# Kernel optimization log

Measured on AMD Instinct MI355X. Metric: run time of the kernel, lower is better.

## Reference

```python
import jax, jax.numpy as jnp
import numpy as np

D_MODEL = 1024
H = 16
D_K = D_MODEL // H


def setup_inputs() -> dict:
    key = jax.random.key(0)
    ks = jax.random.split(key, 11)
    B, S = 4, 2048
    scale = 1.0 / np.sqrt(D_MODEL)
    inp = {
        "q": jax.random.normal(ks[0], (B, S, D_MODEL), jnp.float32),
        "k": jax.random.normal(ks[1], (B, S, D_MODEL), jnp.float32),
        "v": jax.random.normal(ks[2], (B, S, D_MODEL), jnp.float32),
        "wq": jax.random.normal(ks[3], (D_MODEL, D_MODEL), jnp.float32) * scale,
        "bq": jax.random.normal(ks[4], (D_MODEL,), jnp.float32) * 0.02,
        "wk": jax.random.normal(ks[5], (D_MODEL, D_MODEL), jnp.float32) * scale,
        "bk": jax.random.normal(ks[6], (D_MODEL,), jnp.float32) * 0.02,
        "wv": jax.random.normal(ks[7], (D_MODEL, D_MODEL), jnp.float32) * scale,
        "bv": jax.random.normal(ks[8], (D_MODEL,), jnp.float32) * 0.02,
        "wo": jax.random.normal(ks[9], (D_MODEL, D_MODEL), jnp.float32) * scale,
        "bo": jax.random.normal(ks[10], (D_MODEL,), jnp.float32) * 0.02,
    }
    return inp


def _split_heads(x):
    b, s, d = x.shape
    return x.reshape(b, s, H, D_K).transpose(0, 2, 1, 3)  # b h s k


def reference(q, k, v, wq, bq, wk, bk, wv, bv, wo, bo):
    # linear projections (torch Linear: x @ W^T + b; here weights stored as [in,out])
    qh = _split_heads(q @ wq + bq)
    kh = _split_heads(k @ wk + bk)
    vh = _split_heads(v @ wv + bv)
    scores = jnp.einsum('bhsk,bhtk->bhst', qh, kh) / np.sqrt(D_K)
    attn = jax.nn.softmax(scores, axis=-1)
    wv_ = jnp.einsum('bhst,bhtk->bhsk', attn, vh)
    b, h, s, dk = wv_.shape
    cv = wv_.transpose(0, 2, 1, 3).reshape(b, s, h * dk)
    return cv @ wo + bo
```

## Files before the change

kernel.cpp:

```cpp
#include <hip/hip_runtime.h>


#define DM 1024
#define SQL 2048

typedef __attribute__((ext_vector_type(4))) float floatx4;
typedef __attribute__((ext_vector_type(16))) float floatx16;
typedef __attribute__((ext_vector_type(8))) __bf16 bf16x8;
typedef __attribute__((ext_vector_type(4))) __bf16 bf16x4;

#define SW(row, chunk) (((row) << 6) + ((((chunk) ^ ((row) & 7))) << 3))

#define GLD(gaddr, laddr)                                                              \
  __builtin_amdgcn_global_load_lds(                                                    \
      (const __attribute__((address_space(1))) unsigned int*)(gaddr),                  \
      (__attribute__((address_space(3))) unsigned int*)(laddr), 16, 0, 0)

__device__ __forceinline__ unsigned short f2bf(float f) {
  unsigned int u = __float_as_uint(f);
  u += 0x7fffu + ((u >> 16) & 1u);
  return (unsigned short)(u >> 16);
}

__device__ __forceinline__ unsigned int pack_bf(float lo, float hi) {
  unsigned int a = __float_as_uint(lo) + 0x8000u;
  unsigned int b = __float_as_uint(hi) + 0x8000u;
  return __builtin_amdgcn_perm(b, a, 0x07060302u);
}

__global__ __launch_bounds__(256) void transpose4_kernel(
    const float* __restrict__ w0, const float* __restrict__ w1,
    const float* __restrict__ w2, const float* __restrict__ w3,
    unsigned short* __restrict__ t0, unsigned short* __restrict__ t1,
    unsigned short* __restrict__ t2, unsigned short* __restrict__ t3) {
  __shared__ unsigned short t[64][65];
  int z = blockIdx.z;
  const float* W = (z == 0) ? w0 : (z == 1) ? w1 : (z == 2) ? w2 : w3;
  unsigned short* Wt = (z == 0) ? t0 : (z == 1) ? t1 : (z == 2) ? t2 : t3;
  int tid = threadIdx.x;
  int n0 = blockIdx.x * 64, k0 = blockIdx.y * 64;
  for (int u = 0; u < 16; u++) {
    int idx = u * 256 + tid;
    int k = idx >> 6, n = idx & 63;
    t[k][n] = f2bf(W[(size_t)(k0 + k) * DM + n0 + n]);
  }
  __syncthreads();
  for (int u = 0; u < 16; u++) {
    int idx = u * 256 + tid;
    int n = idx >> 6, k = idx & 63;
    Wt[(size_t)(n0 + n) * DM + k0 + k] = t[k][n];
  }
}

__global__ __launch_bounds__(256) void convert3_kernel(
    const float* __restrict__ s0, const float* __restrict__ s1,
    const float* __restrict__ s2, unsigned short* __restrict__ d0,
    unsigned short* __restrict__ d1, unsigned short* __restrict__ d2) {
  int z = blockIdx.y;
  const float* S = (z == 0) ? s0 : (z == 1) ? s1 : s2;
  unsigned short* D = (z == 0) ? d0 : (z == 1) ? d1 : d2;
  int t = blockIdx.x * 256 + threadIdx.x;
  for (int u = 0; u < 8; u++) {
    int i = (u << 18) + t;
    float4 vv = ((const float4*)S)[i];
    uint2 p;
    p.x = pack_bf(vv.x, vv.y);
    p.y = pack_bf(vv.z, vv.w);
    ((uint2*)D)[i] = p;
  }
}

__device__ __forceinline__ void gemm_core_256x128(
    const unsigned short* __restrict__ A, const unsigned short* __restrict__ Bt,
    int m0, int n0, unsigned short* lds_a, unsigned short* lds_b,
    floatx4 acc[4][4]) {
  int tid = threadIdx.x;
  int wave = tid >> 6, lane = tid & 63;
  int quad = lane >> 4, c16 = lane & 15;
  int wm = wave >> 1, wn = wave & 1;
  int r8 = lane >> 3, l8 = lane & 7;
  int xch = (l8 ^ r8) << 3;

  int r7 = c16 & 7;
  int aoff0 = ((wm * 64 + c16) << 6) + ((quad ^ r7) << 3);
  int aoff1 = ((wm * 64 + c16) << 6) + (((4 + quad) ^ r7) << 3);
  int boff0 = ((wn * 64 + c16) << 6) + ((quad ^ r7) << 3);
  int boff1 = ((wn * 64 + c16) << 6) + (((4 + quad) ^ r7) << 3);

  int aq = wave * 4;
  int bq = wave * 2;

#define STG_A(bufp, kt, u) \
  GLD(&A[(size_t)(m0 + (aq + (u)) * 8 + r8) * DM + (kt) + xch], (bufp) + (aq + (u)) * 512)
#define STG_B(bufp, kt, u) \
  GLD(&Bt[(size_t)(n0 + (bq + (u)) * 8 + r8) * DM + (kt) + xch], (bufp) + (bq + (u)) * 512)

  const floatx4 fz = {0.f, 0.f, 0.f, 0.f};
#pragma unroll
  for (int i = 0; i < 4; i++)
#pragma unroll
    for (int j = 0; j < 4; j++) acc[i][j] = fz;

#pragma unroll
  for (int u = 0; u < 4; u++) STG_A(lds_a, 0, u);
  STG_B(lds_b, 0, 0);
  STG_B(lds_b, 0, 1);
#pragma unroll
  for (int u = 0; u < 4; u++) STG_A(lds_a + 16384, 64, u);
  STG_B(lds_b + 8192, 64, 0);
  STG_B(lds_b + 8192, 64, 1);

  int cur = 0;
#pragma unroll 1
  for (int t = 0; t < 16; ++t) {
    if (t < 15) asm volatile("s_waitcnt vmcnt(6)\n\ts_barrier" ::: "memory");
    else        asm volatile("s_waitcnt vmcnt(0)\n\ts_barrier" ::: "memory");

    const unsigned short* la = lds_a + cur * 16384;
    const unsigned short* lb = lds_b + cur * 8192;
    int stg = cur + 2;
    if (stg >= 3) stg -= 3;
    unsigned short* sa = lds_a + stg * 16384;
    unsigned short* sb = lds_b + stg * 8192;
    bool do_st = (t < 14);
    int kt2 = (t + 2) << 6;

    bf16x8 a_[2], b0[4], b1[4];

    a_[0] = *(const bf16x8*)&la[aoff0];
    a_[1] = *(const bf16x8*)&la[aoff0 + 1024];
    b0[0] = *(const bf16x8*)&lb[boff0];
    b0[1] = *(const bf16x8*)&lb[boff0 + 1024];
    b0[2] = *(const bf16x8*)&lb[boff0 + 2048];
    b0[3] = *(const bf16x8*)&lb[boff0 + 3072];
    if (do_st) { STG_A(sa, kt2, 0); STG_A(sa, kt2, 1); }
    __builtin_amdgcn_s_barrier();
    __builtin_amdgcn_s_setprio(1);
#pragma unroll
    for (int j = 0; j < 4; j++)
      acc[0][j] = __builtin_amdgcn_mfma_f32_16x16x32_bf16(a_[0], b0[j], acc[0][j], 0, 0, 0);
#pragma unroll
    for (int j = 0; j < 4; j++)
      acc[1][j] = __builtin_amdgcn_mfma_f32_16x16x32_bf16(a_[1], b0[j], acc[1][j], 0, 0, 0);
    __builtin_amdgcn_s_setprio(0);
    __builtin_amdgcn_s_barrier();

    a_[0] = *(const bf16x8*)&la[aoff0 + 2048];
    a_[1] = *(const bf16x8*)&la[aoff0 + 3072];
    if (do_st) { STG_A(sa, kt2, 2); STG_A(sa, kt2, 3); }
    __builtin_amdgcn_s_barrier();
    __builtin_amdgcn_s_setprio(1);
#pragma unroll
    for (int j = 0; j < 4; j++)
      acc[2][j] = __builtin_amdgcn_mfma_f32_16x16x32_bf16(a_[0], b0[j], acc[2][j], 0, 0, 0);
#pragma unroll
    for (int j = 0; j < 4; j++)
      acc[3][j] = __builtin_amdgcn_mfma_f32_16x16x32_bf16(a_[1], b0[j], acc[3][j], 0, 0, 0);
    __builtin_amdgcn_s_setprio(0);
    __builtin_amdgcn_s_barrier();

    a_[0] = *(const bf16x8*)&la[aoff1];
    a_[1] = *(const bf16x8*)&la[aoff1 + 1024];
    b1[0] = *(const bf16x8*)&lb[boff1];
    b1[1] = *(const bf16x8*)&lb[boff1 + 1024];
    b1[2] = *(const bf16x8*)&lb[boff1 + 2048];
    b1[3] = *(const bf16x8*)&lb[boff1 + 3072];
    if (do_st) { STG_B(sb, kt2, 0); STG_B(sb, kt2, 1); }
    __builtin_amdgcn_s_barrier();
    __builtin_amdgcn_s_setprio(1);
#pragma unroll
    for (int j = 0; j < 4; j++)
      acc[0][j] = __builtin_amdgcn_mfma_f32_16x16x32_bf16(a_[0], b1[j], acc[0][j], 0, 0, 0);
#pragma unroll
    for (int j = 0; j < 4; j++)
      acc[1][j] = __builtin_amdgcn_mfma_f32_16x16x32_bf16(a_[1], b1[j], acc[1][j], 0, 0, 0);
    __builtin_amdgcn_s_setprio(0);
    __builtin_amdgcn_s_barrier();

    a_[0] = *(const bf16x8*)&la[aoff1 + 2048];
    a_[1] = *(const bf16x8*)&la[aoff1 + 3072];
    __builtin_amdgcn_s_barrier();
    __builtin_amdgcn_s_setprio(1);
#pragma unroll
    for (int j = 0; j < 4; j++)
      acc[2][j] = __builtin_amdgcn_mfma_f32_16x16x32_bf16(a_[0], b1[j], acc[2][j], 0, 0, 0);
#pragma unroll
    for (int j = 0; j < 4; j++)
      acc[3][j] = __builtin_amdgcn_mfma_f32_16x16x32_bf16(a_[1], b1[j], acc[3][j], 0, 0, 0);
    __builtin_amdgcn_s_setprio(0);

    cur = cur + 1;
    if (cur >= 3) cur = 0;
  }
#undef STG_A
#undef STG_B
}

__global__ __launch_bounds__(512, 2) void gemm_qkv_kernel(
    const unsigned short* __restrict__ Aq, const unsigned short* __restrict__ Ak,
    const unsigned short* __restrict__ Av, const unsigned short* __restrict__ wqt,
    const unsigned short* __restrict__ wkt, const unsigned short* __restrict__ wvt,
    const float* __restrict__ bq, const float* __restrict__ bk,
    const float* __restrict__ bv, unsigned short* __restrict__ Qb,
    unsigned short* __restrict__ Kb, unsigned short* __restrict__ VtOut,
    float qscale) {
  __shared__ unsigned short lds_a[3 * 256 * 64];
  __shared__ unsigned short lds_b[3 * 128 * 64];

  int lin = blockIdx.x + (blockIdx.y << 3) + (blockIdx.z << 8);
  int swz = (lin & 7) * 96 + (lin >> 3);
  int z = swz >> 8, rem = swz & 255;
  int m0 = (rem >> 3) << 8;
  int n0 = (rem & 7) << 7;

  const unsigned short* A  = (z == 0) ? Aq : (z == 1) ? Ak : Av;
  const unsigned short* Bt = (z == 0) ? wqt : (z == 1) ? wkt : wvt;
  const float* bias = (z == 0) ? bq : (z == 1) ? bk : bv;

  floatx4 acc[4][4];
  gemm_core_256x128(A, Bt, m0, n0, lds_a, lds_b, acc);

  int tid = threadIdx.x;
  int wave = tid >> 6, lane = tid & 63;
  int quad = lane >> 4, c16 = lane & 15;
  int wm = wave >> 1, wn = wave & 1;

  float scale = (z == 0) ? qscale : 1.0f;
#pragma unroll
  for (int i = 0; i < 4; i++)
#pragma unroll
    for (int j = 0; j < 4; j++) {
      int gc = n0 + wn * 64 + j * 16 + c16;
      float bvv = bias[gc];
      float val[4];
#pragma unroll
      for (int r = 0; r < 4; r++) val[r] = (acc[i][j][r] + bvv) * scale;
      int gr0 = m0 + wm * 64 + i * 16 + quad * 4;
      if (z < 2) {
        unsigned short* O = (z == 0) ? Qb : Kb;
#pragma unroll
        for (int r = 0; r < 4; r++) O[(size_t)(gr0 + r) * DM + gc] = f2bf(val[r]);
      } else {
        int hh = gc >> 6, dd = gc & 63;
        int bidx = gr0 >> 11, srow = gr0 & 2047;
        int s6 = srow & 63;
        int c6 = (s6 & 51) | ((s6 & 4) << 1) | ((s6 & 8) >> 1);
        int srowp = (srow & ~63) | c6;
        uint2 pk;
        pk.x = pack_bf(val[0], val[1]);
        pk.y = pack_bf(val[2], val[3]);
        *(uint2*)&VtOut[((size_t)(bidx * 16 + hh) * 64 + dd) * SQL + srowp] = pk;
      }
    }
}

__global__ __launch_bounds__(512, 2) void gemm_out_kernel(
    const unsigned short* __restrict__ A, const unsigned short* __restrict__ Bt,
    const float* __restrict__ bias, float* __restrict__ O) {
  __shared__ unsigned short lds_a[3 * 256 * 64];
  __shared__ unsigned short lds_b[3 * 128 * 64];

  int lin = blockIdx.x + (blockIdx.y << 3);
  int swz = (lin & 7) * 32 + (lin >> 3);
  int m0 = (swz >> 3) << 8;
  int n0 = (swz & 7) << 7;

  floatx4 acc[4][4];
  gemm_core_256x128(A, Bt, m0, n0, lds_a, lds_b, acc);

  int tid = threadIdx.x;
  int wave = tid >> 6, lane = tid & 63;
  int quad = lane >> 4, c16 = lane & 15;
  int wm = wave >> 1, wn = wave & 1;

#pragma unroll
  for (int i = 0; i < 4; i++)
#pragma unroll
    for (int j = 0; j < 4; j++) {
      int gc = n0 + wn * 64 + j * 16 + c16;
      float bvv = bias[gc];
      int gr0 = m0 + wm * 64 + i * 16 + quad * 4;
#pragma unroll
      for (int r = 0; r < 4; r++) O[(size_t)(gr0 + r) * DM + gc] = acc[i][j][r] + bvv;
    }
}

__global__ __launch_bounds__(256, 3) void attn_kernel(
    const unsigned short* __restrict__ Qb, const unsigned short* __restrict__ Kb,
    const unsigned short* __restrict__ Vt, unsigned short* __restrict__ Cv) {
  __shared__ unsigned short lds_k[2][64 * 64];
  __shared__ unsigned short lds_v[2][64 * 64];
  int tid = threadIdx.x;
  int wave = tid >> 6, lane = tid & 63;
  int q31 = lane & 31, hl = lane >> 5;
  int bh = blockIdx.x, qt = blockIdx.y;
  int b = bh >> 4, h = bh & 15;

  int rl = lane >> 3;
  int xsl = ((lane & 7) ^ rl) << 3;
  const unsigned short* kg = &Kb[(size_t)(b * SQL + wave * 16 + rl) * DM + h * 64 + xsl];
  const unsigned short* vg = &Vt[((size_t)(bh * 64) + wave * 16 + rl) * SQL + xsl];

  bf16x8 qf[4];
  int gr = b * SQL + qt * 128 + wave * 32 + q31;
#pragma unroll
  for (int s = 0; s < 4; s++)
    qf[s] = *(const bf16x8*)&Qb[(size_t)gr * DM + h * 64 + s * 16 + hl * 8];

  const floatx16 fz16 = {0.f, 0.f, 0.f, 0.f, 0.f, 0.f, 0.f, 0.f,
                         0.f, 0.f, 0.f, 0.f, 0.f, 0.f, 0.f, 0.f};
  floatx16 o[2];
  o[0] = fz16; o[1] = fz16;
  float l_ = 0.f;

#pragma unroll
  for (int u = 0; u < 2; u++) {
    GLD(kg + (size_t)(u * 8) * DM, &lds_k[0][(wave * 16 + u * 8) << 6]);
    GLD(vg + (size_t)(u * 8) * SQL, &lds_v[0][(wave * 16 + u * 8) << 6]);
  }
  __syncthreads();

#pragma unroll 1
  for (int t = 0; t < 32; t++) {
    int cur = t & 1, nxt = cur ^ 1;
    if (t + 1 < 32) {
      size_t koff = (size_t)((t + 1) * 64) * DM;
      size_t voff = (size_t)((t + 1) * 64);
#pragma unroll
      for (int u = 0; u < 2; u++) {
        GLD(kg + koff + (size_t)(u * 8) * DM, &lds_k[nxt][(wave * 16 + u * 8) << 6]);
        GLD(vg + voff + (size_t)(u * 8) * SQL, &lds_v[nxt][(wave * 16 + u * 8) << 6]);
      }
    }

    floatx16 st[2];
    __builtin_amdgcn_s_setprio(1);
#pragma unroll
    for (int j = 0; j < 2; j++) {
      bf16x8 kf = *(const bf16x8*)&lds_k[cur][SW(j * 32 + q31, hl)];
      st[j] = __builtin_amdgcn_mfma_f32_32x32x16_bf16(kf, qf[0], fz16, 0, 0, 0);
    }
#pragma unroll
    for (int s = 1; s < 4; s++)
#pragma unroll
      for (int j = 0; j < 2; j++) {
        bf16x8 kf = *(const bf16x8*)&lds_k[cur][SW(j * 32 + q31, 2 * s + hl)];
        st[j] = __builtin_amdgcn_mfma_f32_32x32x16_bf16(kf, qf[s], st[j], 0, 0, 0);
      }
    __builtin_amdgcn_s_setprio(0);

#pragma unroll
    for (int j = 0; j < 2; j++)
#pragma unroll
      for (int r = 0; r < 16; r++) st[j][r] = __builtin_amdgcn_exp2f(st[j][r]);
    float p0 = 0.f, p1 = 0.f, p2 = 0.f, p3 = 0.f;
#pragma unroll
    for (int r = 0; r < 16; r += 2) {
      p0 += st[0][r]; p1 += st[0][r + 1];
      p2 += st[1][r]; p3 += st[1][r + 1];
    }
    l_ += (p0 + p1) + (p2 + p3);

    bf16x8 pb[2][2];
#pragma unroll
    for (int j = 0; j < 2; j++)
#pragma unroll
      for (int s2 = 0; s2 < 2; s2++) {
        bf16x8 r;
#pragma unroll
        for (int e = 0; e < 8; e++) r[e] = (__bf16)st[j][s2 * 8 + e];
        pb[j][s2] = r;
      }

    __builtin_amdgcn_s_setprio(1);
#pragma unroll
    for (int dt = 0; dt < 2; dt++)
#pragma unroll
      for (int j = 0; j < 2; j++)
#pragma unroll
        for (int s2 = 0; s2 < 2; s2++) {
          bf16x8 av = *(const bf16x8*)&lds_v[cur][SW(dt * 32 + q31, j * 4 + s2 * 2 + hl)];
          o[dt] = __builtin_amdgcn_mfma_f32_32x32x16_bf16(av, pb[j][s2], o[dt], 0, 0, 0);
        }
    __builtin_amdgcn_s_setprio(0);

    __syncthreads();
  }

  l_ += __shfl_xor(l_, 32);
  float inv = 1.f / l_;
#pragma unroll
  for (int dt = 0; dt < 2; dt++)
#pragma unroll
    for (int g = 0; g < 4; g++) {
      bf16x4 ov;
      ov[0] = (__bf16)(o[dt][4 * g + 0] * inv);
      ov[1] = (__bf16)(o[dt][4 * g + 1] * inv);
      ov[2] = (__bf16)(o[dt][4 * g + 2] * inv);
      ov[3] = (__bf16)(o[dt][4 * g + 3] * inv);
      int d0 = dt * 32 + g * 8 + hl * 4;
      *(bf16x4*)&Cv[(size_t)gr * DM + h * 64 + d0] = ov;
    }
}

extern "C" void kernel_launch(void* const* d_in, const int* in_sizes, int n_in,
                              void* d_out, int out_size, void* d_ws, size_t ws_size,
                              hipStream_t stream) {
  const float* q  = (const float*)d_in[0];
  const float* k  = (const float*)d_in[1];
  const float* v  = (const float*)d_in[2];
  const float* wq = (const float*)d_in[3];
  const float* bq = (const float*)d_in[4];
  const float* wk = (const float*)d_in[5];
  const float* bk = (const float*)d_in[6];
  const float* wv = (const float*)d_in[7];
  const float* bv = (const float*)d_in[8];
  const float* wo = (const float*)d_in[9];
  const float* bo = (const float*)d_in[10];
  float* out = (float*)d_out;

  char* ws = (char*)d_ws;
  unsigned short* wqt = (unsigned short*)(ws + (size_t)0);
  unsigned short* wkt = (unsigned short*)(ws + ((size_t)2 << 20));
  unsigned short* wvt = (unsigned short*)(ws + ((size_t)4 << 20));
  unsigned short* wot = (unsigned short*)(ws + ((size_t)6 << 20));
  unsigned short* Qb  = (unsigned short*)(ws + ((size_t)8 << 20));
  unsigned short* Kb  = (unsigned short*)(ws + ((size_t)24 << 20));
  unsigned short* Vt  = (unsigned short*)(ws + ((size_t)40 << 20));
  unsigned short* Cv  = (unsigned short*)(ws + ((size_t)56 << 20));
  unsigned short* Aq = (unsigned short*)d_out;
  unsigned short* Ak = (unsigned short*)d_out + ((size_t)8 << 20);
  unsigned short* Av = Cv;

  const float QSCALE = 0.125f * 1.44269504088896340736f;

  dim3 blk(256);
  transpose4_kernel<<<dim3(16, 16, 4), blk, 0, stream>>>(wq, wk, wv, wo, wqt, wkt, wvt, wot);
  convert3_kernel<<<dim3(1024, 3), blk, 0, stream>>>(q, k, v, Aq, Ak, Av);
  gemm_qkv_kernel<<<dim3(8, 32, 3), dim3(512), 0, stream>>>(Aq, Ak, Av, wqt, wkt, wvt,
                                                            bq, bk, bv, Qb, Kb, Vt, QSCALE);
  attn_kernel<<<dim3(64, 16), blk, 0, stream>>>(Qb, Kb, Vt, Cv);
  gemm_out_kernel<<<dim3(8, 32), dim3(512), 0, stream>>>(Cv, wot, bo, out);
}
```

Measured before the change: 342.7 us.

## Fuse fp32-to-bf16 input conversion into QKV projection GEMM A-tile loads

Drops the separate convert3 kernel. The QKV GEMM now reads fp32 activations straight into registers, packs them to bf16 and writes them into a double-buffered swizzled LDS tile. The weight tiles still use async global-to-LDS loads with triple buffering. The main loop is restructured to one barrier per K step with prefetch into registers, which removes a full extra read and write pass over the inputs and one launch. In exchange the A loads become register-staged instead of direct-to-LDS, so register pressure rises and each A tile reads twice as many fp32 bytes from global memory.

```diff
diff --git a/kernel.cpp b/kernel.cpp
--- a/kernel.cpp
+++ b/kernel.cpp
@@ -52,28 +52,27 @@
   }
 }
 
-__global__ __launch_bounds__(256) void convert3_kernel(
-    const float* __restrict__ s0, const float* __restrict__ s1,
-    const float* __restrict__ s2, unsigned short* __restrict__ d0,
-    unsigned short* __restrict__ d1, unsigned short* __restrict__ d2) {
-  int z = blockIdx.y;
-  const float* S = (z == 0) ? s0 : (z == 1) ? s1 : s2;
-  unsigned short* D = (z == 0) ? d0 : (z == 1) ? d1 : d2;
-  int t = blockIdx.x * 256 + threadIdx.x;
-  for (int u = 0; u < 8; u++) {
-    int i = (u << 18) + t;
-    float4 vv = ((const float4*)S)[i];
-    uint2 p;
-    p.x = pack_bf(vv.x, vv.y);
-    p.y = pack_bf(vv.z, vv.w);
-    ((uint2*)D)[i] = p;
-  }
-}
-
-__device__ __forceinline__ void gemm_core_256x128(
-    const unsigned short* __restrict__ A, const unsigned short* __restrict__ Bt,
-    int m0, int n0, unsigned short* lds_a, unsigned short* lds_b,
-    floatx4 acc[4][4]) {
+__global__ __launch_bounds__(512, 2) void gemm_qkv_kernel(
+    const float* __restrict__ qf32, const float* __restrict__ kf32,
+    const float* __restrict__ vf32, const unsigned short* __restrict__ wqt,
+    const unsigned short* __restrict__ wkt, const unsigned short* __restrict__ wvt,
+    const float* __restrict__ bq, const float* __restrict__ bk,
+    const float* __restrict__ bv, unsigned short* __restrict__ Qb,
+    unsigned short* __restrict__ Kb, unsigned short* __restrict__ VtOut,
+    float qscale) {
+  __shared__ unsigned short lds_a[2 * 256 * 64];
+  __shared__ unsigned short lds_b[3 * 128 * 64];
+
+  int lin = blockIdx.x + (blockIdx.y << 3) + (blockIdx.z << 8);
+  int swz = (lin & 7) * 96 + (lin >> 3);
+  int z = swz >> 8, rem = swz & 255;
+  int m0 = (rem >> 3) << 8;
+  int n0 = (rem & 7) << 7;
+
+  const float* A = (z == 0) ? qf32 : (z == 1) ? kf32 : vf32;
+  const unsigned short* Bt = (z == 0) ? wqt : (z == 1) ? wkt : wvt;
+  const float* bias = (z == 0) ? bq : (z == 1) ? bk : bv;
+
   int tid = threadIdx.x;
   int wave = tid >> 6, lane = tid & 63;
   int quad = lane >> 4, c16 = lane & 15;
@@ -87,143 +86,127 @@
   int boff0 = ((wn * 64 + c16) << 6) + ((quad ^ r7) << 3);
   int boff1 = ((wn * 64 + c16) << 6) + (((4 + quad) ^ r7) << 3);
 
-  int aq = wave * 4;
-  int bq = wave * 2;
-
-#define STG_A(bufp, kt, u) \
-  GLD(&A[(size_t)(m0 + (aq + (u)) * 8 + r8) * DM + (kt) + xch], (bufp) + (aq + (u)) * 512)
-#define STG_B(bufp, kt, u) \
-  GLD(&Bt[(size_t)(n0 + (bq + (u)) * 8 + r8) * DM + (kt) + xch], (bufp) + (bq + (u)) * 512)
+  int arow = lane >> 4;
+  int acol4 = (c16) * 4;
+  const float* agp = &A[(size_t)(m0 + wave * 32 + arow) * DM + acol4];
+  int cw = c16 >> 1;
+  int awbase = ((wave * 32 + arow) << 6) + ((lane & 1) << 2);
+
+  int bq_ = wave * 2;
+#define STG_B(bufi, kt, u) \
+  GLD(&Bt[(size_t)(n0 + (bq_ + (u)) * 8 + r8) * DM + (kt) + xch], \
+      lds_b + (bufi) * 8192 + (bq_ + (u)) * 512)
+
+#define A_ISSUE(AR, TT)                                                                \
+  _Pragma("unroll") for (int u_ = 0; u_ < 8; u_++)                                     \
+      AR[u_] = *(const float4*)(agp + (size_t)(u_ * 4) * DM + ((TT) << 6));
+#define A_WRITE(AR, BUFI)                                                              \
+  _Pragma("unroll") for (int u_ = 0; u_ < 8; u_++) {                                   \
+    int r7u_ = (arow + ((u_ & 1) << 2)) & 7;                                           \
+    uint2 pw_;                                                                         \
+    pw_.x = pack_bf(AR[u_].x, AR[u_].y);                                               \
+    pw_.y = pack_bf(AR[u_].z, AR[u_].w);                                               \
+    *(uint2*)&lds_a[(BUFI) * 16384 + awbase + u_ * 256 + ((cw ^ r7u_) << 3)] = pw_;    \
+  }
 
   const floatx4 fz = {0.f, 0.f, 0.f, 0.f};
+  floatx4 acc[4][4];
 #pragma unroll
   for (int i = 0; i < 4; i++)
 #pragma unroll
     for (int j = 0; j < 4; j++) acc[i][j] = fz;
 
-#pragma unroll
-  for (int u = 0; u < 4; u++) STG_A(lds_a, 0, u);
-  STG_B(lds_b, 0, 0);
-  STG_B(lds_b, 0, 1);
-#pragma unroll
-  for (int u = 0; u < 4; u++) STG_A(lds_a + 16384, 64, u);
-  STG_B(lds_b + 8192, 64, 0);
-  STG_B(lds_b + 8192, 64, 1);
-
-  int cur = 0;
+  float4 areg[8];
+  A_ISSUE(areg, 0);
+  STG_B(0, 0, 0); STG_B(0, 0, 1);
+  STG_B(1, 64, 0); STG_B(1, 64, 1);
+  asm volatile("s_waitcnt vmcnt(4)" ::: "memory");
+  A_WRITE(areg, 0);
+  asm volatile("s_waitcnt vmcnt(2) lgkmcnt(0)" ::: "memory");
+  __builtin_amdgcn_s_barrier();
+
 #pragma unroll 1
   for (int t = 0; t < 16; ++t) {
-    if (t < 15) asm volatile("s_waitcnt vmcnt(6)\n\ts_barrier" ::: "memory");
-    else        asm volatile("s_waitcnt vmcnt(0)\n\ts_barrier" ::: "memory");
-
-    const unsigned short* la = lds_a + cur * 16384;
-    const unsigned short* lb = lds_b + cur * 8192;
-    int stg = cur + 2;
-    if (stg >= 3) stg -= 3;
-    unsigned short* sa = lds_a + stg * 16384;
-    unsigned short* sb = lds_b + stg * 8192;
-    bool do_st = (t < 14);
-    int kt2 = (t + 2) << 6;
-
-    bf16x8 a_[2], b0[4], b1[4];
-
-    a_[0] = *(const bf16x8*)&la[aoff0];
-    a_[1] = *(const bf16x8*)&la[aoff0 + 1024];
-    b0[0] = *(const bf16x8*)&lb[boff0];
-    b0[1] = *(const bf16x8*)&lb[boff0 + 1024];
-    b0[2] = *(const bf16x8*)&lb[boff0 + 2048];
-    b0[3] = *(const bf16x8*)&lb[boff0 + 3072];
-    if (do_st) { STG_A(sa, kt2, 0); STG_A(sa, kt2, 1); }
-    __builtin_amdgcn_s_barrier();
-    __builtin_amdgcn_s_setprio(1);
-#pragma unroll
-    for (int j = 0; j < 4; j++)
-      acc[0][j] = __builtin_amdgcn_mfma_f32_16x16x32_bf16(a_[0], b0[j], acc[0][j], 0, 0, 0);
-#pragma unroll
-    for (int j = 0; j < 4; j++)
-      acc[1][j] = __builtin_amdgcn_mfma_f32_16x16x32_bf16(a_[1], b0[j], acc[1][j], 0, 0, 0);
-    __builtin_amdgcn_s_setprio(0);
-    __builtin_amdgcn_s_barrier();
-
-    a_[0] = *(const bf16x8*)&la[aoff0 + 2048];
-    a_[1] = *(const bf16x8*)&la[aoff0 + 3072];
-    if (do_st) { STG_A(sa, kt2, 2); STG_A(sa, kt2, 3); }
-    __builtin_amdgcn_s_barrier();
-    __builtin_amdgcn_s_setprio(1);
-#pragma unroll
-    for (int j = 0; j < 4; j++)
-      acc[2][j] = __builtin_amdgcn_mfma_f32_16x16x32_bf16(a_[0], b0[j], acc[2][j], 0, 0, 0);
-#pragma unroll
-    for (int j = 0; j < 4; j++)
-      acc[3][j] = __builtin_amdgcn_mfma_f32_16x16x32_bf16(a_[1], b0[j], acc[3][j], 0, 0, 0);
-    __builtin_amdgcn_s_setprio(0);
-    __builtin_amdgcn_s_barrier();
-
-    a_[0] = *(const bf16x8*)&la[aoff1];
-    a_[1] = *(const bf16x8*)&la[aoff1 + 1024];
-    b1[0] = *(const bf16x8*)&lb[boff1];
-    b1[1] = *(const bf16x8*)&lb[boff1 + 1024];
-    b1[2] = *(const bf16x8*)&lb[boff1 + 2048];
-    b1[3] = *(const bf16x8*)&lb[boff1 + 3072];
-    if (do_st) { STG_B(sb, kt2, 0); STG_B(sb, kt2, 1); }
-    __builtin_amdgcn_s_barrier();
-    __builtin_amdgcn_s_setprio(1);
-#pragma unroll
-    for (int j = 0; j < 4; j++)
-      acc[0][j] = __builtin_amdgcn_mfma_f32_16x16x32_bf16(a_[0], b1[j], acc[0][j], 0, 0, 0);
-#pragma unroll
-    for (int j = 0; j < 4; j++)
-      acc[1][j] = __builtin_amdgcn_mfma_f32_16x16x32_bf16(a_[1], b1[j], acc[1][j], 0, 0, 0);
-    __builtin_amdgcn_s_setprio(0);
-    __builtin_amdgcn_s_barrier();
-
-    a_[0] = *(const bf16x8*)&la[aoff1 + 2048];
-    a_[1] = *(const bf16x8*)&la[aoff1 + 3072];
-    __builtin_amdgcn_s_barrier();
-    __builtin_amdgcn_s_setprio(1);
-#pragma unroll
-    for (int j = 0; j < 4; j++)
-      acc[2][j] = __builtin_amdgcn_mfma_f32_16x16x32_bf16(a_[0], b1[j], acc[2][j], 0, 0, 0);
-#pragma unroll
-    for (int j = 0; j < 4; j++)
-      acc[3][j] = __builtin_amdgcn_mfma_f32_16x16x32_bf16(a_[1], b1[j], acc[3][j], 0, 0, 0);
-    __builtin_amdgcn_s_setprio(0);
-
-    cur = cur + 1;
-    if (cur >= 3) cur = 0;
-  }
-#undef STG_A
+    if (t + 1 < 16) A_ISSUE(areg, t + 1);
+    if (t + 2 < 16) {
+      int bb = (t + 2) % 3;
+      STG_B(bb, (t + 2) << 6, 0);
+      STG_B(bb, (t + 2) << 6, 1);
+    }
+
+    const unsigned short* la = lds_a + (t & 1) * 16384;
+    const unsigned short* lb = lds_b + (t % 3) * 8192;
+
+    {
+      bf16x8 a0 = *(const bf16x8*)&la[aoff0];
+      bf16x8 a1 = *(const bf16x8*)&la[aoff0 + 1024];
+      bf16x8 a2 = *(const bf16x8*)&la[aoff0 + 2048];
+      bf16x8 a3 = *(const bf16x8*)&la[aoff0 + 3072];
+      bf16x8 b0 = *(const bf16x8*)&lb[boff0];
+      bf16x8 b1 = *(const bf16x8*)&lb[boff0 + 1024];
+      bf16x8 b2 = *(const bf16x8*)&lb[boff0 + 2048];
+      bf16x8 b3 = *(const bf16x8*)&lb[boff0 + 3072];
+      __builtin_amdgcn_s_setprio(1);
+      acc[0][0] = __builtin_amdgcn_mfma_f32_16x16x32_bf16(a0, b0, acc[0][0], 0, 0, 0);
+      acc[0][1] = __builtin_amdgcn_mfma_f32_16x16x32_bf16(a0, b1, acc[0][1], 0, 0, 0);
+      acc[0][2] = __builtin_amdgcn_mfma_f32_16x16x32_bf16(a0, b2, acc[0][2], 0, 0, 0);
+      acc[0][3] = __builtin_amdgcn_mfma_f32_16x16x32_bf16(a0, b3, acc[0][3], 0, 0, 0);
+      acc[1][0] = __builtin_amdgcn_mfma_f32_16x16x32_bf16(a1, b0, acc[1][0], 0, 0, 0);
+      acc[1][1] = __builtin_amdgcn_mfma_f32_16x16x32_bf16(a1, b1, acc[1][1], 0, 0, 0);
+      acc[1][2] = __builtin_amdgcn_mfma_f32_16x16x32_bf16(a1, b2, acc[1][2], 0, 0, 0);
+      acc[1][3] = __builtin_amdgcn_mfma_f32_16x16x32_bf16(a1, b3, acc[1][3], 0, 0, 0);
+      acc[2][0] = __builtin_amdgcn_mfma_f32_16x16x32_bf16(a2, b0, acc[2][0], 0, 0, 0);
+      acc[2][1] = __builtin_amdgcn_mfma_f32_16x16x32_bf16(a2, b1, acc[2][1], 0, 0, 0);
+      acc[2][2] = __builtin_amdgcn_mfma_f32_16x16x32_bf16(a2, b2, acc[2][2], 0, 0, 0);
+      acc[2][3] = __builtin_amdgcn_mfma_f32_16x16x32_bf16(a2, b3, acc[2][3], 0, 0, 0);
+      acc[3][0] = __builtin_amdgcn_mfma_f32_16x16x32_bf16(a3, b0, acc[3][0], 0, 0, 0);
+      acc[3][1] = __builtin_amdgcn_mfma_f32_16x16x32_bf16(a3, b1, acc[3][1], 0, 0, 0);
+      acc[3][2] = __builtin_amdgcn_mfma_f32_16x16x32_bf16(a3, b2, acc[3][2], 0, 0, 0);
+      acc[3][3] = __builtin_amdgcn_mfma_f32_16x16x32_bf16(a3, b3, acc[3][3], 0, 0, 0);
+      __builtin_amdgcn_s_setprio(0);
+    }
+    {
+      bf16x8 a0 = *(const bf16x8*)&la[aoff1];
+      bf16x8 a1 = *(const bf16x8*)&la[aoff1 + 1024];
+      bf16x8 a2 = *(const bf16x8*)&la[aoff1 + 2048];
+      bf16x8 a3 = *(const bf16x8*)&la[aoff1 + 3072];
+      bf16x8 b0 = *(const bf16x8*)&lb[boff1];
+      bf16x8 b1 = *(const bf16x8*)&lb[boff1 + 1024];
+      bf16x8 b2 = *(const bf16x8*)&lb[boff1 + 2048];
+      bf16x8 b3 = *(const bf16x8*)&lb[boff1 + 3072];
+      __builtin_amdgcn_s_setprio(1);
+      acc[0][0] = __builtin_amdgcn_mfma_f32_16x16x32_bf16(a0, b0, acc[0][0], 0, 0, 0);
+      acc[0][1] = __builtin_amdgcn_mfma_f32_16x16x32_bf16(a0, b1, acc[0][1], 0, 0, 0);
+      acc[0][2] = __builtin_amdgcn_mfma_f32_16x16x32_bf16(a0, b2, acc[0][2], 0, 0, 0);
+      acc[0][3] = __builtin_amdgcn_mfma_f32_16x16x32_bf16(a0, b3, acc[0][3], 0, 0, 0);
+      acc[1][0] = __builtin_amdgcn_mfma_f32_16x16x32_bf16(a1, b0, acc[1][0], 0, 0, 0);
+      acc[1][1] = __builtin_amdgcn_mfma_f32_16x16x32_bf16(a1, b1, acc[1][1], 0, 0, 0);
+      acc[1][2] = __builtin_amdgcn_mfma_f32_16x16x32_bf16(a1, b2, acc[1][2], 0, 0, 0);
+      acc[1][3] = __builtin_amdgcn_mfma_f32_16x16x32_bf16(a1, b3, acc[1][3], 0, 0, 0);
+      acc[2][0] = __builtin_amdgcn_mfma_f32_16x16x32_bf16(a2, b0, acc[2][0], 0, 0, 0);
+      acc[2][1] = __builtin_amdgcn_mfma_f32_16x16x32_bf16(a2, b1, acc[2][1], 0, 0, 0);
+      acc[2][2] = __builtin_amdgcn_mfma_f32_16x16x32_bf16(a2, b2, acc[2][2], 0, 0, 0);
+      acc[2][3] = __builtin_amdgcn_mfma_f32_16x16x32_bf16(a2, b3, acc[2][3], 0, 0, 0);
+      acc[3][0] = __builtin_amdgcn_mfma_f32_16x16x32_bf16(a3, b0, acc[3][0], 0, 0, 0);
+      acc[3][1] = __builtin_amdgcn_mfma_f32_16x16x32_bf16(a3, b1, acc[3][1], 0, 0, 0);
+      acc[3][2] = __builtin_amdgcn_mfma_f32_16x16x32_bf16(a3, b2, acc[3][2], 0, 0, 0);
+      acc[3][3] = __builtin_amdgcn_mfma_f32_16x16x32_bf16(a3, b3, acc[3][3], 0, 0, 0);
+      __builtin_amdgcn_s_setprio(0);
+    }
+
+    if (t + 1 < 16) {
+      if (t + 2 < 16) asm volatile("s_waitcnt vmcnt(2)" ::: "memory");
+      else            asm volatile("s_waitcnt vmcnt(0)" ::: "memory");
+      A_WRITE(areg, (t + 1) & 1);
+    }
+    if (t + 1 < 16) {
+      asm volatile("s_waitcnt lgkmcnt(0)" ::: "memory");
+      __builtin_amdgcn_s_barrier();
+    }
+  }
 #undef STG_B
-}
-
-__global__ __launch_bounds__(512, 2) void gemm_qkv_kernel(
-    const unsigned short* __restrict__ Aq, const unsigned short* __restrict__ Ak,
-    const unsigned short* __restrict__ Av, const unsigned short* __restrict__ wqt,
-    const unsigned short* __restrict__ wkt, const unsigned short* __restrict__ wvt,
-    const float* __restrict__ bq, const float* __restrict__ bk,
-    const float* __restrict__ bv, unsigned short* __restrict__ Qb,
-    unsigned short* __restrict__ Kb, unsigned short* __restrict__ VtOut,
-    float qscale) {
-  __shared__ unsigned short lds_a[3 * 256 * 64];
-  __shared__ unsigned short lds_b[3 * 128 * 64];
-
-  int lin = blockIdx.x + (blockIdx.y << 3) + (blockIdx.z << 8);
-  int swz = (lin & 7) * 96 + (lin >> 3);
-  int z = swz >> 8, rem = swz & 255;
-  int m0 = (rem >> 3) << 8;
-  int n0 = (rem & 7) << 7;
-
-  const unsigned short* A  = (z == 0) ? Aq : (z == 1) ? Ak : Av;
-  const unsigned short* Bt = (z == 0) ? wqt : (z == 1) ? wkt : wvt;
-  const float* bias = (z == 0) ? bq : (z == 1) ? bk : bv;
-
-  floatx4 acc[4][4];
-  gemm_core_256x128(A, Bt, m0, n0, lds_a, lds_b, acc);
-
-  int tid = threadIdx.x;
-  int wave = tid >> 6, lane = tid & 63;
-  int quad = lane >> 4, c16 = lane & 15;
-  int wm = wave >> 1, wn = wave & 1;
+#undef A_ISSUE
+#undef A_WRITE
 
   float scale = (z == 0) ? qscale : 1.0f;
 #pragma unroll
@@ -252,6 +235,132 @@
         *(uint2*)&VtOut[((size_t)(bidx * 16 + hh) * 64 + dd) * SQL + srowp] = pk;
       }
     }
+}
+
+__device__ __forceinline__ void gemm_core_256x128(
+    const unsigned short* __restrict__ A, const unsigned short* __restrict__ Bt,
+    int m0, int n0, unsigned short* lds_a, unsigned short* lds_b,
+    floatx4 acc[4][4]) {
+  int tid = threadIdx.x;
+  int wave = tid >> 6, lane = tid & 63;
+  int quad = lane >> 4, c16 = lane & 15;
+  int wm = wave >> 1, wn = wave & 1;
+  int r8 = lane >> 3, l8 = lane & 7;
+  int xch = (l8 ^ r8) << 3;
+
+  int r7 = c16 & 7;
+  int aoff0 = ((wm * 64 + c16) << 6) + ((quad ^ r7) << 3);
+  int aoff1 = ((wm * 64 + c16) << 6) + (((4 + quad) ^ r7) << 3);
+  int boff0 = ((wn * 64 + c16) << 6) + ((quad ^ r7) << 3);
+  int boff1 = ((wn * 64 + c16) << 6) + (((4 + quad) ^ r7) << 3);
+
+  int aq = wave * 4;
+  int bq = wave * 2;
+
+#define STG_A(bufp, kt, u) \
+  GLD(&A[(size_t)(m0 + (aq + (u)) * 8 + r8) * DM + (kt) + xch], (bufp) + (aq + (u)) * 512)
+#define STG_B(bufp, kt, u) \
+  GLD(&Bt[(size_t)(n0 + (bq + (u)) * 8 + r8) * DM + (kt) + xch], (bufp) + (bq + (u)) * 512)
+
+  const floatx4 fz = {0.f, 0.f, 0.f, 0.f};
+#pragma unroll
+  for (int i = 0; i < 4; i++)
+#pragma unroll
+    for (int j = 0; j < 4; j++) acc[i][j] = fz;
+
+#pragma unroll
+  for (int u = 0; u < 4; u++) STG_A(lds_a, 0, u);
+  STG_B(lds_b, 0, 0);
+  STG_B(lds_b, 0, 1);
+#pragma unroll
+  for (int u = 0; u < 4; u++) STG_A(lds_a + 16384, 64, u);
+  STG_B(lds_b + 8192, 64, 0);
+  STG_B(lds_b + 8192, 64, 1);
+
+  int cur = 0;
+#pragma unroll 1
+  for (int t = 0; t < 16; ++t) {
+    if (t < 15) asm volatile("s_waitcnt vmcnt(6)\n\ts_barrier" ::: "memory");
+    else        asm volatile("s_waitcnt vmcnt(0)\n\ts_barrier" ::: "memory");
+
+    const unsigned short* la = lds_a + cur * 16384;
+    const unsigned short* lb = lds_b + cur * 8192;
+    int stg = cur + 2;
+    if (stg >= 3) stg -= 3;
+    unsigned short* sa = lds_a + stg * 16384;
+    unsigned short* sb = lds_b + stg * 8192;
+    bool do_st = (t < 14);
+    int kt2 = (t + 2) << 6;
+
+    bf16x8 a_[2], b0[4], b1[4];
+
+    a_[0] = *(const bf16x8*)&la[aoff0];
+    a_[1] = *(const bf16x8*)&la[aoff0 + 1024];
+    b0[0] = *(const bf16x8*)&lb[boff0];
+    b0[1] = *(const bf16x8*)&lb[boff0 + 1024];
+    b0[2] = *(const bf16x8*)&lb[boff0 + 2048];
+    b0[3] = *(const bf16x8*)&lb[boff0 + 3072];
+    if (do_st) { STG_A(sa, kt2, 0); STG_A(sa, kt2, 1); }
+    __builtin_amdgcn_s_barrier();
+    __builtin_amdgcn_s_setprio(1);
+#pragma unroll
+    for (int j = 0; j < 4; j++)
+      acc[0][j] = __builtin_amdgcn_mfma_f32_16x16x32_bf16(a_[0], b0[j], acc[0][j], 0, 0, 0);
+#pragma unroll
+    for (int j = 0; j < 4; j++)
+      acc[1][j] = __builtin_amdgcn_mfma_f32_16x16x32_bf16(a_[1], b0[j], acc[1][j], 0, 0, 0);
+    __builtin_amdgcn_s_setprio(0);
+    __builtin_amdgcn_s_barrier();
+
+    a_[0] = *(const bf16x8*)&la[aoff0 + 2048];
+    a_[1] = *(const bf16x8*)&la[aoff0 + 3072];
+    if (do_st) { STG_A(sa, kt2, 2); STG_A(sa, kt2, 3); }
+    __builtin_amdgcn_s_barrier();
+    __builtin_amdgcn_s_setprio(1);
+#pragma unroll
+    for (int j = 0; j < 4; j++)
+      acc[2][j] = __builtin_amdgcn_mfma_f32_16x16x32_bf16(a_[0], b0[j], acc[2][j], 0, 0, 0);
+#pragma unroll
+    for (int j = 0; j < 4; j++)
+      acc[3][j] = __builtin_amdgcn_mfma_f32_16x16x32_bf16(a_[1], b0[j], acc[3][j], 0, 0, 0);
+    __builtin_amdgcn_s_setprio(0);
+    __builtin_amdgcn_s_barrier();
+
+    a_[0] = *(const bf16x8*)&la[aoff1];
+    a_[1] = *(const bf16x8*)&la[aoff1 + 1024];
+    b1[0] = *(const bf16x8*)&lb[boff1];
+    b1[1] = *(const bf16x8*)&lb[boff1 + 1024];
+    b1[2] = *(const bf16x8*)&lb[boff1 + 2048];
+    b1[3] = *(const bf16x8*)&lb[boff1 + 3072];
+    if (do_st) { STG_B(sb, kt2, 0); STG_B(sb, kt2, 1); }
+    __builtin_amdgcn_s_barrier();
+    __builtin_amdgcn_s_setprio(1);
+#pragma unroll
+    for (int j = 0; j < 4; j++)
+      acc[0][j] = __builtin_amdgcn_mfma_f32_16x16x32_bf16(a_[0], b1[j], acc[0][j], 0, 0, 0);
+#pragma unroll
+    for (int j = 0; j < 4; j++)
+      acc[1][j] = __builtin_amdgcn_mfma_f32_16x16x32_bf16(a_[1], b1[j], acc[1][j], 0, 0, 0);
+    __builtin_amdgcn_s_setprio(0);
+    __builtin_amdgcn_s_barrier();
+
+    a_[0] = *(const bf16x8*)&la[aoff1 + 2048];
+    a_[1] = *(const bf16x8*)&la[aoff1 + 3072];
+    __builtin_amdgcn_s_barrier();
+    __builtin_amdgcn_s_setprio(1);
+#pragma unroll
+    for (int j = 0; j < 4; j++)
+      acc[2][j] = __builtin_amdgcn_mfma_f32_16x16x32_bf16(a_[0], b1[j], acc[2][j], 0, 0, 0);
+#pragma unroll
+    for (int j = 0; j < 4; j++)
+      acc[3][j] = __builtin_amdgcn_mfma_f32_16x16x32_bf16(a_[1], b1[j], acc[3][j], 0, 0, 0);
+    __builtin_amdgcn_s_setprio(0);
+
+    cur = cur + 1;
+    if (cur >= 3) cur = 0;
+  }
+#undef STG_A
+#undef STG_B
 }
 
 __global__ __launch_bounds__(512, 2) void gemm_out_kernel(
@@ -428,16 +537,12 @@
   unsigned short* Kb  = (unsigned short*)(ws + ((size_t)24 << 20));
   unsigned short* Vt  = (unsigned short*)(ws + ((size_t)40 << 20));
   unsigned short* Cv  = (unsigned short*)(ws + ((size_t)56 << 20));
-  unsigned short* Aq = (unsigned short*)d_out;
-  unsigned short* Ak = (unsigned short*)d_out + ((size_t)8 << 20);
-  unsigned short* Av = Cv;
 
   const float QSCALE = 0.125f * 1.44269504088896340736f;
 
   dim3 blk(256);
   transpose4_kernel<<<dim3(16, 16, 4), blk, 0, stream>>>(wq, wk, wv, wo, wqt, wkt, wvt, wot);
-  convert3_kernel<<<dim3(1024, 3), blk, 0, stream>>>(q, k, v, Aq, Ak, Av);
-  gemm_qkv_kernel<<<dim3(8, 32, 3), dim3(512), 0, stream>>>(Aq, Ak, Av, wqt, wkt, wvt,
+  gemm_qkv_kernel<<<dim3(8, 32, 3), dim3(512), 0, stream>>>(q, k, v, wqt, wkt, wvt,
                                                             bq, bk, bv, Qb, Kb, Vt, QSCALE);
   attn_kernel<<<dim3(64, 16), blk, 0, stream>>>(Qb, Kb, Vt, Cv);
   gemm_out_kernel<<<dim3(8, 32), dim3(512), 0, stream>>>(Cv, wot, bo, out);
```

Result: slower. 377.8 us (+10.2%).
